# Optimization experiments

Measured on AMD Instinct MI355X. Metric: run time of the kernel, lower is better.

Reference implementation:

```python
import jax, jax.numpy as jnp
import numpy as np

NUM_HEADS = 8
HEAD_DIM = 64  # joiner_dim 512 / 8
LN_EPS = 1e-5


def _layer_norm(x, g, b):
    mu = jnp.mean(x, axis=-1, keepdims=True)
    var = jnp.mean(jnp.square(x - mu), axis=-1, keepdims=True)
    return (x - mu) * jax.lax.rsqrt(var + LN_EPS) * g + b


def setup_inputs() -> dict:
    key = jax.random.key(0)
    ks = jax.random.split(key, 24)
    N, T, S = 16, 512, 5
    E, D, J, V = 512, 512, 512, 2000
    s = 0.02
    inp = {
        "encoder_out": jax.random.normal(ks[0], (N, T, S, E), jnp.float32),
        "decoder_out": jax.random.normal(ks[1], (N, T, S, D), jnp.float32),
        # ScaledLinear projections (initial_scale absorbed into weights)
        "We": jax.random.normal(ks[2], (J, E), jnp.float32) * s * 0.25,
        "be": jnp.zeros((J,), jnp.float32),
        "Wd": jax.random.normal(ks[3], (J, D), jnp.float32) * s * 0.25,
        "bd": jnp.zeros((J,), jnp.float32),
        # LayerNorms
        "g_q": jnp.ones((J,), jnp.float32),
        "beta_q": jnp.zeros((J,), jnp.float32),
        "g_kv": jnp.ones((J,), jnp.float32),
        "beta_kv": jnp.zeros((J,), jnp.float32),
        # attention projections (xavier-ish)
        "Wq": jax.random.normal(ks[4], (J, J), jnp.float32) * s,
        "bq": jnp.zeros((J,), jnp.float32),
        "Wk": jax.random.normal(ks[5], (J, J), jnp.float32) * s,
        "bk": jnp.zeros((J,), jnp.float32),
        "Wv": jax.random.normal(ks[6], (J, J), jnp.float32) * s,
        "bv": jnp.zeros((J,), jnp.float32),
        "Wo": jax.random.normal(ks[7], (J, J), jnp.float32) * s,
        "bo": jnp.zeros((J,), jnp.float32),
        # final vocab projection
        "Wout": jax.random.normal(ks[8], (V, J), jnp.float32) * s,
        "bout": jnp.zeros((V,), jnp.float32),
    }
    return inp


def reference(encoder_out, decoder_out, We, be, Wd, bd, g_q, beta_q, g_kv, beta_kv,
              Wq, bq, Wk, bk, Wv, bv, Wo, bo, Wout, bout):
    # input projections (mode == "transducer", project_input=True)
    enc = jnp.einsum('ntsc,jc->ntsj', encoder_out, We) + be
    dec = jnp.einsum('ntsc,jc->ntsj', decoder_out, Wd) + bd

    # framewise sigmoid attention
    q_in = _layer_norm(dec, g_q, beta_q)
    kv_in = _layer_norm(enc, g_kv, beta_kv)
    q = jnp.einsum('ntsj,kj->ntsk', q_in, Wq) + bq
    k = jnp.einsum('ntsj,kj->ntsk', kv_in, Wk) + bk
    v = jnp.einsum('ntsj,kj->ntsk', kv_in, Wv) + bv

    shp = q.shape[:-1]
    q = q.reshape(*shp, NUM_HEADS, HEAD_DIM)
    k = k.reshape(*shp, NUM_HEADS, HEAD_DIM)
    v = v.reshape(*shp, NUM_HEADS, HEAD_DIM)

    scale = HEAD_DIM ** -0.5
    attn = jax.nn.sigmoid(jnp.sum(q * k, axis=-1, keepdims=True) * scale)  # (N,T,S,H,1)
    context = (attn * v).reshape(*shp, NUM_HEADS * HEAD_DIM)
    context = jnp.einsum('ntsj,kj->ntsk', context, Wo) + bo

    h = jnp.tanh(dec + context)
    logits = jnp.einsum('ntsj,vj->ntsv', h, Wout) + bout
    return logits
```

## Files before the change

### kernel.cpp

```cpp
#include <hip/hip_runtime.h>
#include <stdint.h>


typedef __attribute__((ext_vector_type(8))) __bf16 bf16x8;
typedef __attribute__((ext_vector_type(4))) float float4v;
typedef __attribute__((ext_vector_type(8))) unsigned short ushort8;

static constexpr int M_TOT = 16 * 512 * 5;
static constexpr int JDIM  = 512;
static constexpr int VOUT  = 2000;
static constexpr int VPAD  = 2048;

#define DI __device__ __forceinline__

DI float bf2f(unsigned short u) {
    union { unsigned int i; float f; } w; w.i = ((unsigned int)u) << 16; return w.f;
}
DI unsigned short f2bf(float f) {
    union { float f; unsigned int i; } w; w.f = f;
    return (unsigned short)((w.i + 0x8000u) >> 16);
}

DI void gld_lds16(const void* g, void* l) {
    __builtin_amdgcn_global_load_lds(
        reinterpret_cast<__attribute__((address_space(1))) void*>(
            reinterpret_cast<uintptr_t>(g)),
        reinterpret_cast<__attribute__((address_space(3))) void*>(
            reinterpret_cast<uintptr_t>(l)),
        16, 0, 0);
}

template <int EPI, int NOUT, bool SWZ>
__global__ __launch_bounds__(256) void gemm_bt(
    const unsigned short* __restrict__ A, const unsigned short* __restrict__ B,
    const float* __restrict__ bias, void* __restrict__ Cp,
    const unsigned short* __restrict__ dres,
    float* __restrict__ st_sum, float* __restrict__ st_ssq,
    const float* __restrict__ rs)
{
    constexpr int K = 512;
    constexpr int BM = 128, BN = 128, BK = 32;
    __shared__ unsigned short As[BM * BK];
    __shared__ unsigned short Bs[BN * BK];

    const int tid  = threadIdx.x;
    const int wave = tid >> 6;
    const int lane = tid & 63;
    const int wm   = wave >> 1;
    const int wn   = wave & 1;
    const int quad = lane >> 4;
    const int l16  = lane & 15;

    const int gx = gridDim.x;
    const int id = blockIdx.x + gx * blockIdx.y;
    int logical;
    if constexpr (SWZ) {
        const int nwg = gx * gridDim.y;
        logical = (id & 7) * (nwg >> 3) + (id >> 3);
    } else {
        logical = id;
    }
    const int m0 = (logical / gx) * BM;
    const int n0 = (logical % gx) * BN;

    float4v acc[4][4];
#pragma unroll
    for (int i = 0; i < 4; i++)
#pragma unroll
        for (int j = 0; j < 4; j++)
            acc[i][j] = {0.f, 0.f, 0.f, 0.f};

    const int c0 = tid, c1 = tid + 256;
    const int ar0 = c0 >> 2, ac0 = (c0 & 3) * 8;
    const int ar1 = c1 >> 2, ac1 = (c1 & 3) * 8;

    for (int k0 = 0; k0 < K; k0 += BK) {
        gld_lds16(&B[(size_t)(n0 + ar0) * K + k0 + ac0], &Bs[c0 * 8]);
        gld_lds16(&B[(size_t)(n0 + ar1) * K + k0 + ac1], &Bs[c1 * 8]);
        gld_lds16(&A[(size_t)(m0 + ar0) * K + k0 + ac0], &As[c0 * 8]);
        gld_lds16(&A[(size_t)(m0 + ar1) * K + k0 + ac1], &As[c1 * 8]);
        __syncthreads();

        bf16x8 af[4], bfv[4];
#pragma unroll
        for (int i = 0; i < 4; i++)
            af[i] = *reinterpret_cast<const bf16x8*>(
                &As[(wm * 64 + i * 16 + l16) * BK + quad * 8]);
#pragma unroll
        for (int j = 0; j < 4; j++)
            bfv[j] = *reinterpret_cast<const bf16x8*>(
                &Bs[(wn * 64 + j * 16 + l16) * BK + quad * 8]);
#pragma unroll
        for (int i = 0; i < 4; i++)
#pragma unroll
            for (int j = 0; j < 4; j++)
                acc[i][j] = __builtin_amdgcn_mfma_f32_16x16x32_bf16(
                    af[i], bfv[j], acc[i][j], 0, 0, 0);
        __syncthreads();
    }

    float bias_v[4], rs_v[4];
#pragma unroll
    for (int j = 0; j < 4; j++) {
        int col = n0 + wn * 64 + j * 16 + l16;
        bias_v[j] = (col < NOUT) ? bias[col] : 0.f;
        if constexpr (EPI == 4) rs_v[j] = rs[col];
    }

    if constexpr (EPI == 4) {
#pragma unroll
        for (int i = 0; i < 4; i++) {
            int rbase = m0 + wm * 64 + i * 16 + quad * 4;
#pragma unroll
            for (int r = 0; r < 4; r++) {
                int row = rbase + r;
                float s  = st_sum[row];
                float s2 = st_ssq[row];
                float mean = s * (1.f / 512.f);
                float var  = s2 * (1.f / 512.f) - mean * mean;
                float rstd = rsqrtf(var + 1e-5f);
                float crow = -mean * rstd;
#pragma unroll
                for (int j = 0; j < 4; j++) {
                    int col = n0 + wn * 64 + j * 16 + l16;
                    float val = fmaf(rstd, acc[i][j][r],
                                fmaf(crow, rs_v[j], bias_v[j]));
                    ((unsigned short*)Cp)[(size_t)row * NOUT + col] = f2bf(val);
                }
            }
        }
    } else {
#pragma unroll
        for (int i = 0; i < 4; i++) {
            int rbase = m0 + wm * 64 + i * 16 + quad * 4;
#pragma unroll
            for (int j = 0; j < 4; j++) {
                int col = n0 + wn * 64 + j * 16 + l16;
#pragma unroll
                for (int r = 0; r < 4; r++) {
                    float val = acc[i][j][r] + bias_v[j];
                    int row = rbase + r;
                    if constexpr (EPI == 2) {
                        float d = bf2f(dres[(size_t)row * 512 + col]);
                        ((unsigned short*)Cp)[(size_t)row * 512 + col] = f2bf(tanhf(d + val));
                    } else if constexpr (EPI == 3) {
                        if (col < NOUT)
                            ((float*)Cp)[(size_t)row * NOUT + col] = val;
                    } else {
                        ((unsigned short*)Cp)[(size_t)row * NOUT + col] = f2bf(val);
                    }
                }
            }
        }
    }

    if constexpr (EPI == 6) {
#pragma unroll
        for (int i = 0; i < 4; i++) {
#pragma unroll
            for (int r = 0; r < 4; r++) {
                float ps = 0.f, ps2 = 0.f;
#pragma unroll
                for (int j = 0; j < 4; j++) {
                    float v = acc[i][j][r] + bias_v[j];
                    ps += v;
                    ps2 = fmaf(v, v, ps2);
                }
#pragma unroll
                for (int m = 1; m < 16; m <<= 1) {
                    ps  += __shfl_xor(ps,  m, 64);
                    ps2 += __shfl_xor(ps2, m, 64);
                }
                if (l16 == 0) {
                    int row = m0 + wm * 64 + i * 16 + quad * 4 + r;
                    atomicAdd(&st_sum[row], ps);
                    atomicAdd(&st_ssq[row], ps2);
                }
            }
        }
    }
}

__global__ __launch_bounds__(256) void prep_kernel(
    const float* __restrict__ We, const float* __restrict__ Wd,
    const float* __restrict__ Wq, const float* __restrict__ Wk,
    const float* __restrict__ Wv, const float* __restrict__ Wo,
    const float* __restrict__ Wout,
    const float* __restrict__ g_q, const float* __restrict__ beta_q,
    const float* __restrict__ g_kv, const float* __restrict__ beta_kv,
    const float* __restrict__ bq, const float* __restrict__ bk,
    const float* __restrict__ bv,
    const float* __restrict__ enc_in, const float* __restrict__ dec_in,
    unsigned short* __restrict__ WB,
    unsigned short* __restrict__ encB, unsigned short* __restrict__ decB,
    float* __restrict__ stz,
    float* __restrict__ rs_q, float* __restrict__ b_q,
    float* __restrict__ rs_kv, float* __restrict__ b_kv)
{
    const int b   = blockIdx.x;
    const int tid = threadIdx.x;

    if (b < 1280) {
        if (b < 768) {
            const int seg = b >> 7;
            const int off = (b & 127) * 2048 + tid * 8;
            const float* src = seg == 0 ? We : seg == 1 ? Wd : seg == 2 ? Wq
                             : seg == 3 ? Wk : seg == 4 ? Wv : Wo;
            float4 f0 = *(const float4*)&src[off];
            float4 f1 = *(const float4*)&src[off + 4];
            float sc[8] = {1,1,1,1,1,1,1,1};
            if (seg >= 2 && seg <= 4) {
                const float* g = (seg == 2) ? g_q : g_kv;
                int j0 = off & 511;
                float4 s0 = *(const float4*)&g[j0];
                float4 s1 = *(const float4*)&g[j0 + 4];
                sc[0]=s0.x; sc[1]=s0.y; sc[2]=s0.z; sc[3]=s0.w;
                sc[4]=s1.x; sc[5]=s1.y; sc[6]=s1.z; sc[7]=s1.w;
            }
            ushort8 u;
            u[0]=f2bf(f0.x*sc[0]); u[1]=f2bf(f0.y*sc[1]); u[2]=f2bf(f0.z*sc[2]); u[3]=f2bf(f0.w*sc[3]);
            u[4]=f2bf(f1.x*sc[4]); u[5]=f2bf(f1.y*sc[5]); u[6]=f2bf(f1.z*sc[6]); u[7]=f2bf(f1.w*sc[7]);
            *reinterpret_cast<ushort8*>(&WB[(size_t)b * 2048 + tid * 8]) = u;
        } else {
            const int rem = (b - 768) * 2048 + tid * 8;
            const int row = rem >> 9;
            ushort8 u;
            if (row < VOUT) {
                float4 f0 = *(const float4*)&Wout[rem];
                float4 f1 = *(const float4*)&Wout[rem + 4];
                u[0]=f2bf(f0.x); u[1]=f2bf(f0.y); u[2]=f2bf(f0.z); u[3]=f2bf(f0.w);
                u[4]=f2bf(f1.x); u[5]=f2bf(f1.y); u[6]=f2bf(f1.z); u[7]=f2bf(f1.w);
            } else {
                u = (ushort8)0;
            }
            *reinterpret_cast<ushort8*>(&WB[1572864 + (size_t)(b - 768) * 2048 + tid * 8]) = u;
        }
        int z = b * 256 + tid;
        if (z < 163840) stz[z] = 0.f;
    } else if (b < 21760) {
        const bool isDec = b >= 11520;
        const int  cb    = b - (isDec ? 11520 : 1280);
        const float* src = isDec ? dec_in : enc_in;
        unsigned short* dst = isDec ? decB : encB;
        const size_t base = (size_t)cb * 2048 + tid * 8;
        float4 f0 = *(const float4*)&src[base];
        float4 f1 = *(const float4*)&src[base + 4];
        ushort8 u;
        u[0]=f2bf(f0.x); u[1]=f2bf(f0.y); u[2]=f2bf(f0.z); u[3]=f2bf(f0.w);
        u[4]=f2bf(f1.x); u[5]=f2bf(f1.y); u[6]=f2bf(f1.z); u[7]=f2bf(f1.w);
        *reinterpret_cast<ushort8*>(&dst[base]) = u;
    } else {
        const int idx  = (b - 21760) * 4 + (tid >> 6);
        const int lane = tid & 63;
        const float *W, *g, *bt, *bb; float *rs_out, *b_out; int r;
        if (idx < 512)       { W = Wq; g = g_q;  bt = beta_q;  bb = bq;
                               rs_out = &rs_q[idx];        b_out = &b_q[idx];        r = idx; }
        else if (idx < 1024) { W = Wk; g = g_kv; bt = beta_kv; bb = bk;
                               rs_out = &rs_kv[idx - 512]; b_out = &b_kv[idx - 512]; r = idx - 512; }
        else                 { W = Wv; g = g_kv; bt = beta_kv; bb = bv;
                               rs_out = &rs_kv[idx - 512]; b_out = &b_kv[idx - 512]; r = idx - 1024; }

        const float* wr = &W[(size_t)r * 512];
        float s = 0.f, sb = 0.f;
        int j0 = lane * 8;
        float4 w0 = *(const float4*)&wr[j0];
        float4 w1 = *(const float4*)&wr[j0 + 4];
        float4 ga = *(const float4*)&g[j0];
        float4 gb = *(const float4*)&g[j0 + 4];
        float4 ba = *(const float4*)&bt[j0];
        float4 bb4 = *(const float4*)&bt[j0 + 4];
        s  += w0.x * ga.x + w0.y * ga.y + w0.z * ga.z + w0.w * ga.w;
        s  += w1.x * gb.x + w1.y * gb.y + w1.z * gb.z + w1.w * gb.w;
        sb += w0.x * ba.x + w0.y * ba.y + w0.z * ba.z + w0.w * ba.w;
        sb += w1.x * bb4.x + w1.y * bb4.y + w1.z * bb4.z + w1.w * bb4.w;
#pragma unroll
        for (int m = 1; m < 64; m <<= 1) {
            s  += __shfl_xor(s,  m, 64);
            sb += __shfl_xor(sb, m, 64);
        }
        if (lane == 0) { *rs_out = s; *b_out = bb[r] + sb; }
    }
}

__global__ __launch_bounds__(256) void attn_kernel(
    const unsigned short* __restrict__ q, const unsigned short* __restrict__ kv,
    unsigned short* __restrict__ ctx)
{
    int row  = blockIdx.x * 4 + (threadIdx.x >> 6);
    int lane = threadIdx.x & 63;
    size_t qoff = (size_t)row * 512 + lane * 8;
    size_t kvo  = (size_t)row * 1024 + lane * 8;
    ushort8 uq = *reinterpret_cast<const ushort8*>(&q[qoff]);
    ushort8 uk = *reinterpret_cast<const ushort8*>(&kv[kvo]);
    float dot = 0.f;
#pragma unroll
    for (int j = 0; j < 8; j++) dot += bf2f(uq[j]) * bf2f(uk[j]);
    dot += __shfl_xor(dot, 1, 64);
    dot += __shfl_xor(dot, 2, 64);
    dot += __shfl_xor(dot, 4, 64);
    float sg = 1.f / (1.f + __expf(-dot * 0.125f));
    ushort8 uv = *reinterpret_cast<const ushort8*>(&kv[kvo + 512]);
    ushort8 o;
#pragma unroll
    for (int j = 0; j < 8; j++) o[j] = f2bf(sg * bf2f(uv[j]));
    *reinterpret_cast<ushort8*>(&ctx[qoff]) = o;
}

extern "C" void kernel_launch(void* const* d_in, const int* in_sizes, int n_in,
                              void* d_out, int out_size, void* d_ws, size_t ws_size,
                              hipStream_t stream)
{
    (void)in_sizes; (void)n_in; (void)out_size; (void)ws_size;
    const float* enc_in  = (const float*)d_in[0];
    const float* dec_in  = (const float*)d_in[1];
    const float* We      = (const float*)d_in[2];  const float* be     = (const float*)d_in[3];
    const float* Wd      = (const float*)d_in[4];  const float* bd     = (const float*)d_in[5];
    const float* g_q     = (const float*)d_in[6];  const float* beta_q = (const float*)d_in[7];
    const float* g_kv    = (const float*)d_in[8];  const float* beta_kv= (const float*)d_in[9];
    const float* Wq      = (const float*)d_in[10]; const float* bq     = (const float*)d_in[11];
    const float* Wk      = (const float*)d_in[12]; const float* bk     = (const float*)d_in[13];
    const float* Wv      = (const float*)d_in[14]; const float* bv     = (const float*)d_in[15];
    const float* Wo      = (const float*)d_in[16]; const float* bo     = (const float*)d_in[17];
    const float* Wout    = (const float*)d_in[18]; const float* bout   = (const float*)d_in[19];
    float* out = (float*)d_out;

    unsigned short* WB    = (unsigned short*)d_ws;
    unsigned short* WeB   = WB + 0;
    unsigned short* WdB   = WB + 262144;
    unsigned short* WqB   = WB + 524288;
    unsigned short* WkB   = WB + 786432;
    unsigned short* WoB   = WB + 1310720;
    unsigned short* WoutB = WB + 1572864;

    char* sbase = (char*)d_ws + 5242880;
    const size_t SZ = (size_t)M_TOT * 512 * 2;
    unsigned short* EB = (unsigned short*)(sbase + 0 * SZ);
    unsigned short* DB = (unsigned short*)(sbase + 1 * SZ);
    unsigned short* S0 = (unsigned short*)(sbase + 2 * SZ);
    unsigned short* S1 = (unsigned short*)(sbase + 3 * SZ);
    unsigned short* S2 = (unsigned short*)(sbase + 4 * SZ);
    unsigned short* S3 = (unsigned short*)(sbase + 5 * SZ);
    unsigned short* S4 = (unsigned short*)(sbase + 6 * SZ);
    unsigned short* S5 = (unsigned short*)(sbase + 7 * SZ);

    float* stf  = (float*)(sbase + 7 * SZ);
    float* sumE = stf;
    float* ssqE = stf + 40960;
    float* sumD = stf + 81920;
    float* ssqD = stf + 122880;
    float* rs_q  = stf + 163840;
    float* b_q   = stf + 164352;
    float* rs_kv = stf + 164864;
    float* b_kv  = stf + 165888;

    dim3 blk(256);
    dim3 g512(JDIM / 128, M_TOT / 128);
    dim3 g1024(1024 / 128, M_TOT / 128);
    dim3 gout(VPAD / 128, M_TOT / 128);

    prep_kernel<<<22144, blk, 0, stream>>>(
        We, Wd, Wq, Wk, Wv, Wo, Wout, g_q, beta_q, g_kv, beta_kv,
        bq, bk, bv, enc_in, dec_in, WB, EB, DB, stf, rs_q, b_q, rs_kv, b_kv);

    gemm_bt<6, 512, false><<<g512, blk, 0, stream>>>(EB, WeB, be, S0, nullptr,
                                                     sumE, ssqE, nullptr);
    gemm_bt<6, 512, false><<<g512, blk, 0, stream>>>(DB, WdB, bd, S1, nullptr,
                                                     sumD, ssqD, nullptr);

    gemm_bt<4, 512, false><<<g512, blk, 0, stream>>>(S1, WqB, b_q, S4, nullptr,
                                                     sumD, ssqD, rs_q);
    gemm_bt<4, 1024, false><<<g1024, blk, 0, stream>>>(S0, WkB, b_kv, S2, nullptr,
                                                       sumE, ssqE, rs_kv);

    attn_kernel<<<M_TOT / 4, blk, 0, stream>>>(S4, S2, S5);

    gemm_bt<2, 512, false><<<g512, blk, 0, stream>>>(S5, WoB, bo, S3, S1,
                                                     nullptr, nullptr, nullptr);

    gemm_bt<3, 2000, true><<<gout, blk, 0, stream>>>(S3, WoutB, bout, out, nullptr,
                                                     nullptr, nullptr, nullptr);
}
```

Before: 916.6 us.

## Fuse input cast into projection GEMMs, merge launches, fold sigmoid-scale into Wo GEMM

Drops the separate fp32-to-bf16 conversion pass over encoder and decoder inputs. The projection GEMMs now read fp32 directly and convert while staging into LDS. The enc/dec projections and the q/kv projections are each merged into a single launch. The attention kernel now writes only per-head sigmoid gates, and the Wo GEMM applies them to V while loading its A tile, which removes the context tensor round trip. The tanh also switches to an exp-based formula. In exchange, the fp32 A loads are synchronous register loads instead of async global-to-LDS copies, and each GEMM re-reads fp32 inputs once per N-tile (4x), so input traffic rises.

```diff
diff --git a/kernel.cpp b/kernel.cpp
--- a/kernel.cpp
+++ b/kernel.cpp
@@ -7,7 +7,6 @@
 typedef __attribute__((ext_vector_type(8))) unsigned short ushort8;
 
 static constexpr int M_TOT = 16 * 512 * 5;
-static constexpr int JDIM  = 512;
 static constexpr int VOUT  = 2000;
 static constexpr int VPAD  = 2048;
 
@@ -30,19 +29,16 @@
         16, 0, 0);
 }
 
-template <int EPI, int NOUT, bool SWZ>
-__global__ __launch_bounds__(256) void gemm_bt(
-    const unsigned short* __restrict__ A, const unsigned short* __restrict__ B,
-    const float* __restrict__ bias, void* __restrict__ Cp,
-    const unsigned short* __restrict__ dres,
-    float* __restrict__ st_sum, float* __restrict__ st_ssq,
-    const float* __restrict__ rs)
-{
-    constexpr int K = 512;
-    constexpr int BM = 128, BN = 128, BK = 32;
-    __shared__ unsigned short As[BM * BK];
-    __shared__ unsigned short Bs[BN * BK];
-
+template <int EPI, int AMODE>
+DI void gemm_core(unsigned short* __restrict__ As, unsigned short* __restrict__ Bs,
+                  const void* __restrict__ Ap, const unsigned short* __restrict__ B,
+                  const float* __restrict__ bias, void* __restrict__ Cp,
+                  int ldC, int nout, int m0, int n0,
+                  const unsigned short* __restrict__ dres,
+                  float* __restrict__ st_sum, float* __restrict__ st_ssq,
+                  const float* __restrict__ rs, const float* __restrict__ sg)
+{
+    constexpr int K = 512, BK = 32;
     const int tid  = threadIdx.x;
     const int wave = tid >> 6;
     const int lane = tid & 63;
@@ -51,18 +47,6 @@
     const int quad = lane >> 4;
     const int l16  = lane & 15;
 
-    const int gx = gridDim.x;
-    const int id = blockIdx.x + gx * blockIdx.y;
-    int logical;
-    if constexpr (SWZ) {
-        const int nwg = gx * gridDim.y;
-        logical = (id & 7) * (nwg >> 3) + (id >> 3);
-    } else {
-        logical = id;
-    }
-    const int m0 = (logical / gx) * BM;
-    const int n0 = (logical % gx) * BN;
-
     float4v acc[4][4];
 #pragma unroll
     for (int i = 0; i < 4; i++)
@@ -77,8 +61,48 @@
     for (int k0 = 0; k0 < K; k0 += BK) {
         gld_lds16(&B[(size_t)(n0 + ar0) * K + k0 + ac0], &Bs[c0 * 8]);
         gld_lds16(&B[(size_t)(n0 + ar1) * K + k0 + ac1], &Bs[c1 * 8]);
-        gld_lds16(&A[(size_t)(m0 + ar0) * K + k0 + ac0], &As[c0 * 8]);
-        gld_lds16(&A[(size_t)(m0 + ar1) * K + k0 + ac1], &As[c1 * 8]);
+        if constexpr (AMODE == 0) {
+            const unsigned short* Ab = (const unsigned short*)Ap;
+            gld_lds16(&Ab[(size_t)(m0 + ar0) * K + k0 + ac0], &As[c0 * 8]);
+            gld_lds16(&Ab[(size_t)(m0 + ar1) * K + k0 + ac1], &As[c1 * 8]);
+        } else if constexpr (AMODE == 1) {
+            const float* Af = (const float*)Ap;
+            const float* p0 = &Af[(size_t)(m0 + ar0) * K + k0 + ac0];
+            const float* p1 = &Af[(size_t)(m0 + ar1) * K + k0 + ac1];
+            float4 f0 = *(const float4*)p0;
+            float4 f1 = *(const float4*)(p0 + 4);
+            float4 g0 = *(const float4*)p1;
+            float4 g1 = *(const float4*)(p1 + 4);
+            ushort8 u0, u1;
+            u0[0] = f2bf(f0.x); u0[1] = f2bf(f0.y); u0[2] = f2bf(f0.z); u0[3] = f2bf(f0.w);
+            u0[4] = f2bf(f1.x); u0[5] = f2bf(f1.y); u0[6] = f2bf(f1.z); u0[7] = f2bf(f1.w);
+            u1[0] = f2bf(g0.x); u1[1] = f2bf(g0.y); u1[2] = f2bf(g0.z); u1[3] = f2bf(g0.w);
+            u1[4] = f2bf(g1.x); u1[5] = f2bf(g1.y); u1[6] = f2bf(g1.z); u1[7] = f2bf(g1.w);
+            *reinterpret_cast<ushort8*>(&As[c0 * 8]) = u0;
+            *reinterpret_cast<ushort8*>(&As[c1 * 8]) = u1;
+        } else {
+            const unsigned short* kvb = (const unsigned short*)Ap;
+            {
+                int row = m0 + ar0;
+                float s = sg[row * 8 + ((k0 + ac0) >> 6)];
+                ushort8 uv = *reinterpret_cast<const ushort8*>(
+                    &kvb[(size_t)row * 1024 + 512 + k0 + ac0]);
+                ushort8 u;
+#pragma unroll
+                for (int j = 0; j < 8; j++) u[j] = f2bf(s * bf2f(uv[j]));
+                *reinterpret_cast<ushort8*>(&As[c0 * 8]) = u;
+            }
+            {
+                int row = m0 + ar1;
+                float s = sg[row * 8 + ((k0 + ac1) >> 6)];
+                ushort8 uv = *reinterpret_cast<const ushort8*>(
+                    &kvb[(size_t)row * 1024 + 512 + k0 + ac1]);
+                ushort8 u;
+#pragma unroll
+                for (int j = 0; j < 8; j++) u[j] = f2bf(s * bf2f(uv[j]));
+                *reinterpret_cast<ushort8*>(&As[c1 * 8]) = u;
+            }
+        }
         __syncthreads();
 
         bf16x8 af[4], bfv[4];
@@ -103,7 +127,7 @@
 #pragma unroll
     for (int j = 0; j < 4; j++) {
         int col = n0 + wn * 64 + j * 16 + l16;
-        bias_v[j] = (col < NOUT) ? bias[col] : 0.f;
+        bias_v[j] = (col < nout) ? bias[col] : 0.f;
         if constexpr (EPI == 4) rs_v[j] = rs[col];
     }
 
@@ -125,7 +149,7 @@
                     int col = n0 + wn * 64 + j * 16 + l16;
                     float val = fmaf(rstd, acc[i][j][r],
                                 fmaf(crow, rs_v[j], bias_v[j]));
-                    ((unsigned short*)Cp)[(size_t)row * NOUT + col] = f2bf(val);
+                    ((unsigned short*)Cp)[(size_t)row * ldC + col] = f2bf(val);
                 }
             }
         }
@@ -141,13 +165,14 @@
                     float val = acc[i][j][r] + bias_v[j];
                     int row = rbase + r;
                     if constexpr (EPI == 2) {
-                        float d = bf2f(dres[(size_t)row * 512 + col]);
-                        ((unsigned short*)Cp)[(size_t)row * 512 + col] = f2bf(tanhf(d + val));
+                        float t = bf2f(dres[(size_t)row * 512 + col]) + val;
+                        float th = 1.f - 2.f / (__expf(t + t) + 1.f);
+                        ((unsigned short*)Cp)[(size_t)row * ldC + col] = f2bf(th);
                     } else if constexpr (EPI == 3) {
-                        if (col < NOUT)
-                            ((float*)Cp)[(size_t)row * NOUT + col] = val;
+                        if (col < nout)
+                            ((float*)Cp)[(size_t)row * ldC + col] = val;
                     } else {
-                        ((unsigned short*)Cp)[(size_t)row * NOUT + col] = f2bf(val);
+                        ((unsigned short*)Cp)[(size_t)row * ldC + col] = f2bf(val);
                     }
                 }
             }
@@ -181,6 +206,79 @@
     }
 }
 
+__global__ __launch_bounds__(256) void k_projED(
+    const float* __restrict__ enc_in, const float* __restrict__ dec_in,
+    const unsigned short* __restrict__ WeB, const unsigned short* __restrict__ WdB,
+    const float* __restrict__ be, const float* __restrict__ bd,
+    unsigned short* __restrict__ S0, unsigned short* __restrict__ S1,
+    float* __restrict__ sumE, float* __restrict__ ssqE,
+    float* __restrict__ sumD, float* __restrict__ ssqD)
+{
+    __shared__ unsigned short As[128 * 32];
+    __shared__ unsigned short Bs[128 * 32];
+    const bool isDec = blockIdx.x >= 4;
+    const int  bx    = blockIdx.x - (isDec ? 4 : 0);
+    gemm_core<6, 1>(As, Bs,
+                    isDec ? (const void*)dec_in : (const void*)enc_in,
+                    isDec ? WdB : WeB, isDec ? bd : be,
+                    isDec ? (void*)S1 : (void*)S0,
+                    512, 512, blockIdx.y * 128, bx * 128,
+                    nullptr,
+                    isDec ? sumD : sumE, isDec ? ssqD : ssqE,
+                    nullptr, nullptr);
+}
+
+__global__ __launch_bounds__(256) void k_qkv(
+    const unsigned short* __restrict__ S1, const unsigned short* __restrict__ S0,
+    const unsigned short* __restrict__ WqB, const unsigned short* __restrict__ WkvB,
+    const float* __restrict__ b_q, const float* __restrict__ b_kv,
+    unsigned short* __restrict__ Sq, unsigned short* __restrict__ Skv,
+    float* __restrict__ sumD, float* __restrict__ ssqD,
+    float* __restrict__ sumE, float* __restrict__ ssqE,
+    const float* __restrict__ rs_q, const float* __restrict__ rs_kv)
+{
+    __shared__ unsigned short As[128 * 32];
+    __shared__ unsigned short Bs[128 * 32];
+    const bool isKV = blockIdx.x >= 4;
+    const int  bx   = blockIdx.x - (isKV ? 4 : 0);
+    gemm_core<4, 0>(As, Bs,
+                    isKV ? (const void*)S0 : (const void*)S1,
+                    isKV ? WkvB : WqB, isKV ? b_kv : b_q,
+                    isKV ? (void*)Skv : (void*)Sq,
+                    isKV ? 1024 : 512, isKV ? 1024 : 512,
+                    blockIdx.y * 128, bx * 128,
+                    nullptr,
+                    isKV ? sumE : sumD, isKV ? ssqE : ssqD,
+                    isKV ? rs_kv : rs_q, nullptr);
+}
+
+__global__ __launch_bounds__(256) void k_ctxo(
+    const unsigned short* __restrict__ kv, const float* __restrict__ sg,
+    const unsigned short* __restrict__ WoB, const float* __restrict__ bo,
+    unsigned short* __restrict__ H, const unsigned short* __restrict__ dres)
+{
+    __shared__ unsigned short As[128 * 32];
+    __shared__ unsigned short Bs[128 * 32];
+    gemm_core<2, 2>(As, Bs, kv, WoB, bo, H, 512, 512,
+                    blockIdx.y * 128, blockIdx.x * 128,
+                    dres, nullptr, nullptr, nullptr, sg);
+}
+
+__global__ __launch_bounds__(256) void k_out(
+    const unsigned short* __restrict__ H, const unsigned short* __restrict__ WoutB,
+    const float* __restrict__ bout, float* __restrict__ out)
+{
+    __shared__ unsigned short As[128 * 32];
+    __shared__ unsigned short Bs[128 * 32];
+    const int gx  = gridDim.x;
+    const int nwg = gx * gridDim.y;
+    const int id  = blockIdx.x + gx * blockIdx.y;
+    const int logical = (id & 7) * (nwg >> 3) + (id >> 3);
+    gemm_core<3, 0>(As, Bs, H, WoutB, bout, out, VOUT, VOUT,
+                    (logical / gx) * 128, (logical % gx) * 128,
+                    nullptr, nullptr, nullptr, nullptr, nullptr);
+}
+
 __global__ __launch_bounds__(256) void prep_kernel(
     const float* __restrict__ We, const float* __restrict__ Wd,
     const float* __restrict__ Wq, const float* __restrict__ Wk,
@@ -190,10 +288,7 @@
     const float* __restrict__ g_kv, const float* __restrict__ beta_kv,
     const float* __restrict__ bq, const float* __restrict__ bk,
     const float* __restrict__ bv,
-    const float* __restrict__ enc_in, const float* __restrict__ dec_in,
-    unsigned short* __restrict__ WB,
-    unsigned short* __restrict__ encB, unsigned short* __restrict__ decB,
-    float* __restrict__ stz,
+    unsigned short* __restrict__ WB, float* __restrict__ stz,
     float* __restrict__ rs_q, float* __restrict__ b_q,
     float* __restrict__ rs_kv, float* __restrict__ b_kv)
 {
@@ -237,20 +332,8 @@
         }
         int z = b * 256 + tid;
         if (z < 163840) stz[z] = 0.f;
-    } else if (b < 21760) {
-        const bool isDec = b >= 11520;
-        const int  cb    = b - (isDec ? 11520 : 1280);
-        const float* src = isDec ? dec_in : enc_in;
-        unsigned short* dst = isDec ? decB : encB;
-        const size_t base = (size_t)cb * 2048 + tid * 8;
-        float4 f0 = *(const float4*)&src[base];
-        float4 f1 = *(const float4*)&src[base + 4];
-        ushort8 u;
-        u[0]=f2bf(f0.x); u[1]=f2bf(f0.y); u[2]=f2bf(f0.z); u[3]=f2bf(f0.w);
-        u[4]=f2bf(f1.x); u[5]=f2bf(f1.y); u[6]=f2bf(f1.z); u[7]=f2bf(f1.w);
-        *reinterpret_cast<ushort8*>(&dst[base]) = u;
     } else {
-        const int idx  = (b - 21760) * 4 + (tid >> 6);
+        const int idx  = (b - 1280) * 4 + (tid >> 6);
         const int lane = tid & 63;
         const float *W, *g, *bt, *bb; float *rs_out, *b_out; int r;
         if (idx < 512)       { W = Wq; g = g_q;  bt = beta_q;  bb = bq;
@@ -282,28 +365,22 @@
     }
 }
 
-__global__ __launch_bounds__(256) void attn_kernel(
+__global__ __launch_bounds__(256) void attnq_kernel(
     const unsigned short* __restrict__ q, const unsigned short* __restrict__ kv,
-    unsigned short* __restrict__ ctx)
+    float* __restrict__ sg)
 {
     int row  = blockIdx.x * 4 + (threadIdx.x >> 6);
     int lane = threadIdx.x & 63;
-    size_t qoff = (size_t)row * 512 + lane * 8;
-    size_t kvo  = (size_t)row * 1024 + lane * 8;
-    ushort8 uq = *reinterpret_cast<const ushort8*>(&q[qoff]);
-    ushort8 uk = *reinterpret_cast<const ushort8*>(&kv[kvo]);
+    ushort8 uq = *reinterpret_cast<const ushort8*>(&q[(size_t)row * 512 + lane * 8]);
+    ushort8 uk = *reinterpret_cast<const ushort8*>(&kv[(size_t)row * 1024 + lane * 8]);
     float dot = 0.f;
 #pragma unroll
     for (int j = 0; j < 8; j++) dot += bf2f(uq[j]) * bf2f(uk[j]);
     dot += __shfl_xor(dot, 1, 64);
     dot += __shfl_xor(dot, 2, 64);
     dot += __shfl_xor(dot, 4, 64);
-    float sg = 1.f / (1.f + __expf(-dot * 0.125f));
-    ushort8 uv = *reinterpret_cast<const ushort8*>(&kv[kvo + 512]);
-    ushort8 o;
-#pragma unroll
-    for (int j = 0; j < 8; j++) o[j] = f2bf(sg * bf2f(uv[j]));
-    *reinterpret_cast<ushort8*>(&ctx[qoff]) = o;
+    if ((lane & 7) == 0)
+        sg[(size_t)row * 8 + (lane >> 3)] = 1.f / (1.f + __expf(-dot * 0.125f));
 }
 
 extern "C" void kernel_launch(void* const* d_in, const int* in_sizes, int n_in,
@@ -328,22 +405,19 @@
     unsigned short* WeB   = WB + 0;
     unsigned short* WdB   = WB + 262144;
     unsigned short* WqB   = WB + 524288;
-    unsigned short* WkB   = WB + 786432;
+    unsigned short* WkvB  = WB + 786432;
     unsigned short* WoB   = WB + 1310720;
     unsigned short* WoutB = WB + 1572864;
 
     char* sbase = (char*)d_ws + 5242880;
     const size_t SZ = (size_t)M_TOT * 512 * 2;
-    unsigned short* EB = (unsigned short*)(sbase + 0 * SZ);
-    unsigned short* DB = (unsigned short*)(sbase + 1 * SZ);
-    unsigned short* S0 = (unsigned short*)(sbase + 2 * SZ);
-    unsigned short* S1 = (unsigned short*)(sbase + 3 * SZ);
-    unsigned short* S2 = (unsigned short*)(sbase + 4 * SZ);
-    unsigned short* S3 = (unsigned short*)(sbase + 5 * SZ);
-    unsigned short* S4 = (unsigned short*)(sbase + 6 * SZ);
-    unsigned short* S5 = (unsigned short*)(sbase + 7 * SZ);
-
-    float* stf  = (float*)(sbase + 7 * SZ);
+    unsigned short* S0 = (unsigned short*)(sbase + 0 * SZ);
+    unsigned short* S1 = (unsigned short*)(sbase + 1 * SZ);
+    unsigned short* S2 = (unsigned short*)(sbase + 2 * SZ);
+    unsigned short* S4 = (unsigned short*)(sbase + 4 * SZ);
+    unsigned short* S5 = (unsigned short*)(sbase + 5 * SZ);
+
+    float* stf  = (float*)S5;
     float* sumE = stf;
     float* ssqE = stf + 40960;
     float* sumD = stf + 81920;
@@ -352,31 +426,24 @@
     float* b_q   = stf + 164352;
     float* rs_kv = stf + 164864;
     float* b_kv  = stf + 165888;
+    float* sg    = stf + 166912;
 
     dim3 blk(256);
-    dim3 g512(JDIM / 128, M_TOT / 128);
-    dim3 g1024(1024 / 128, M_TOT / 128);
-    dim3 gout(VPAD / 128, M_TOT / 128);
-
-    prep_kernel<<<22144, blk, 0, stream>>>(
+
+    prep_kernel<<<1664, blk, 0, stream>>>(
         We, Wd, Wq, Wk, Wv, Wo, Wout, g_q, beta_q, g_kv, beta_kv,
-        bq, bk, bv, enc_in, dec_in, WB, EB, DB, stf, rs_q, b_q, rs_kv, b_kv);
-
-    gemm_bt<6, 512, false><<<g512, blk, 0, stream>>>(EB, WeB, be, S0, nullptr,
-                                                     sumE, ssqE, nullptr);
-    gemm_bt<6, 512, false><<<g512, blk, 0, stream>>>(DB, WdB, bd, S1, nullptr,
-                                                     sumD, ssqD, nullptr);
-
-    gemm_bt<4, 512, false><<<g512, blk, 0, stream>>>(S1, WqB, b_q, S4, nullptr,
-                                                     sumD, ssqD, rs_q);
-    gemm_bt<4, 1024, false><<<g1024, blk, 0, stream>>>(S0, WkB, b_kv, S2, nullptr,
-                                                       sumE, ssqE, rs_kv);
-
-    attn_kernel<<<M_TOT / 4, blk, 0, stream>>>(S4, S2, S5);
-
-    gemm_bt<2, 512, false><<<g512, blk, 0, stream>>>(S5, WoB, bo, S3, S1,
-                                                     nullptr, nullptr, nullptr);
-
-    gemm_bt<3, 2000, true><<<gout, blk, 0, stream>>>(S3, WoutB, bout, out, nullptr,
-                                                     nullptr, nullptr, nullptr);
-}
+        bq, bk, bv, WB, stf, rs_q, b_q, rs_kv, b_kv);
+
+    k_projED<<<dim3(8, 320), blk, 0, stream>>>(
+        enc_in, dec_in, WeB, WdB, be, bd, S0, S1, sumE, ssqE, sumD, ssqD);
+
+    k_qkv<<<dim3(12, 320), blk, 0, stream>>>(
+        S1, S0, WqB, WkvB, b_q, b_kv, S4, S2,
+        sumD, ssqD, sumE, ssqE, rs_q, rs_kv);
+
+    attnq_kernel<<<M_TOT / 4, blk, 0, stream>>>(S4, S2, sg);
+
+    k_ctxo<<<dim3(4, 320), blk, 0, stream>>>(S2, sg, WoB, bo, S4, S1);
+
+    k_out<<<dim3(16, 320), blk, 0, stream>>>(S4, WoutB, bout, out);
+}
```

Result: faster. 871.9 us (-4.9%).
